# Optimization experiments

Hardware: AMD Instinct MI355X
Metric: run time of the kernel (lower is better)

## Reference

```python
import jax, jax.numpy as jnp
import numpy as np

DX = 1.0
DY = 1.0
W_DIV = 1e9
W_SMOOTH = 10.0
W_STD = 100.0
EPS = 1e-10


def _corner(a, i, j, k):
    # slice dims 2,3,4: 0 -> [0:-1], 1 -> [1:]
    sl = lambda b: slice(1, None) if b else slice(0, -1)
    return a[:, :, sl(i), sl(j), sl(k)]


def setup_inputs() -> dict:
    key = jax.random.key(0)
    k1, k2 = jax.random.split(key)
    outputs = jax.random.normal(k1, (2, 1, 256, 256, 64), dtype=jnp.float32)
    targets = jax.random.normal(k2, (2, 3, 256, 256, 64), dtype=jnp.float32)
    return {"outputs": outputs, "targets": targets}


def _loss(outputs, targets):
    bx, by, bz = targets[:, 0:1], targets[:, 1:2], targets[:, 2:3]
    z = outputs[:, 0:1]

    # vertical thickness and smoothness of its square
    dz = z[..., 1:] - z[..., :-1]
    dz2 = dz ** 2
    lap = (6 * dz2[:, :, 1:-1, 1:-1, 1:-1]
           - dz2[:, :, :-2, 1:-1, 1:-1] - dz2[:, :, 2:, 1:-1, 1:-1]
           - dz2[:, :, 1:-1, :-2, 1:-1] - dz2[:, :, 1:-1, 2:, 1:-1]
           - dz2[:, :, 1:-1, 1:-1, 2:] - dz2[:, :, 1:-1, 1:-1, :-2])
    loss_smooth = jnp.mean(lap ** 2)

    # per-(batch, channel, z) std over the spatial plane (unbiased, matching torch.std)
    loss_std = jnp.mean(jnp.std(dz, axis=(2, 3), ddof=1))

    # 8 cell corners for each field
    corners = lambda a: {(i, j, k): _corner(a, i, j, k)
                         for i in (0, 1) for j in (0, 1) for k in (0, 1)}
    BX, BY, BZ, Z = corners(bx), corners(by), corners(bz), corners(z)

    az = lambda a, b: jnp.abs(Z[a] - Z[b])
    num = (0.25 * (BX[1,0,0] + BX[1,1,0] + BX[1,0,1] + BX[1,1,1]) * DY * 0.5 * (az((1,0,1),(1,0,0)) + az((1,1,1),(1,1,0)))
           - 0.25 * (BX[0,0,0] + BX[0,1,0] + BX[0,0,1] + BX[0,1,1]) * DY * 0.5 * (az((0,0,1),(0,0,0)) + az((0,1,1),(0,1,0)))
           + 0.25 * (BY[0,1,0] + BY[1,1,0] + BY[0,1,1] + BY[1,1,1]) * DX * 0.5 * (az((0,1,1),(0,1,0)) + az((1,1,1),(1,1,0)))
           - 0.25 * (BY[0,0,0] + BY[1,0,0] + BY[0,0,1] + BY[1,0,1]) * DX * 0.5 * (az((0,0,1),(0,0,0)) + az((1,0,1),(1,0,0)))
           + 0.25 * (BZ[0,0,1] + BZ[0,1,1] + BZ[1,0,1] + BZ[1,1,1]) * DX * DY
           - 0.25 * (BZ[0,0,0] + BZ[0,1,0] + BZ[1,0,0] + BZ[1,1,0]) * DX * DY
           + (BX[0,0,1] + BX[1,0,1] + BX[1,1,1]) * DY * (Z[0,0,1] - Z[1,0,1]) / 6
           + (BX[0,1,1] + BX[1,1,1] + BX[1,0,1]) * DY * (Z[0,1,1] - Z[1,1,1]) / 6
           + (BY[1,0,1] + BY[1,1,1] + BY[0,1,1]) * DX * (Z[1,0,1] - Z[1,1,1]) / 6
           + (BY[0,0,1] + BY[0,1,1] + BY[1,1,1]) * DX * (Z[0,0,1] - Z[0,1,1]) / 6
           - (BX[0,0,0] + BX[1,0,0] + BX[1,1,0]) * DY * (Z[0,0,0] - Z[1,0,0]) / 6
           - (BX[0,1,0] + BX[1,1,0] + BX[1,0,0]) * DY * (Z[0,1,0] - Z[1,1,0]) / 6
           - (BY[1,0,0] + BY[1,1,0] + BY[0,1,0]) * DX * (Z[1,0,0] - Z[1,1,0]) / 6
           - (BY[0,0,0] + BY[0,1,0] + BY[1,1,0]) * DX * (Z[0,0,0] - Z[0,1,0]) / 6)

    sum8 = lambda C: sum(C.values())
    den = ((sum8(BX) * 0.125) ** 2 + (sum8(BY) * 0.125) ** 2
           + (sum8(BZ) * 0.125) ** 2 + EPS)
    loss_div = jnp.mean(num ** 2 / den)

    return loss_div * W_DIV, loss_smooth * W_SMOOTH + loss_std * W_STD


def reference(outputs, targets):
    return _loss(outputs, targets)
```

## Files before the change

kernel.cpp:

```cpp
#include <hip/hip_runtime.h>
#include <math.h>


__global__ __launch_bounds__(512) void zero_ws_kernel(float* ws) {
    for (int i = threadIdx.x; i < 32 * 258; i += 512) ws[i] = 0.0f;
}

__global__ __launch_bounds__(256, 4) void fused_loss_kernel(
    const float* __restrict__ zin, const float* __restrict__ tg,
    float* __restrict__ ws)
{
    __shared__ float r1[4][64];
    __shared__ float r2[4][64];
    __shared__ float rsc[4][2];

    const int tid  = threadIdx.x;
    const int lane = tid & 63;
    const int w    = tid >> 6;

    const int bb   = blockIdx.x >> 14;
    const int rest = blockIdx.x & 16383;
    const int tx   = rest & 127;
    const int ty   = rest >> 7;
    const int x    = (tx << 1) | (w >> 1);
    const int y    = (ty << 1) | (w & 1);

    const int xp = x < 255 ? x + 1 : 255;
    const int yp = y < 255 ? y + 1 : 255;
    const int xm = x > 0 ? x - 1 : 0;
    const int ym = y > 0 ? y - 1 : 0;

    const int o00 = x  * 16384 + y  * 64 + lane;
    const int o10 = xp * 16384 + y  * 64 + lane;
    const int o01 = x  * 16384 + yp * 64 + lane;
    const int o11 = xp * 16384 + yp * 64 + lane;

    const float* zb = zin + ((size_t)bb << 22);
    float zC  = zb[o00];
    float zE  = zb[o10];
    float zN  = zb[o01];
    float zNE = zb[o11];
    float zW  = zb[xm * 16384 + y * 64 + lane];
    float zS  = zb[x * 16384 + ym * 64 + lane];

    const float* tbx = tg + (((size_t)bb * 3) << 22);
    const float* tby = tbx + 4194304;
    const float* tbz = tbx + 8388608;
    float bx00 = tbx[o00], bx10 = tbx[o10], bx01 = tbx[o01], bx11 = tbx[o11];
    float by00 = tby[o00], by10 = tby[o10], by01 = tby[o01], by11 = tby[o11];
    float bz00 = tbz[o00], bz10 = tbz[o10], bz01 = tbz[o01], bz11 = tbz[o11];

    float zCp  = __shfl_down(zC,  1, 64);
    float zEp  = __shfl_down(zE,  1, 64);
    float zNp  = __shfl_down(zN,  1, 64);
    float zNEp = __shfl_down(zNE, 1, 64);
    float zWp  = __shfl_down(zW,  1, 64);
    float zSp  = __shfl_down(zS,  1, 64);

    float dz   = zCp  - zC;
    float dzE  = zEp  - zE;
    float dzN  = zNp  - zN;
    float dzNE = zNEp - zNE;
    float dzW  = zWp  - zW;
    float dzS  = zSp  - zS;

    float dzm = __shfl_up(dz, 1, 64);
    float dzp = __shfl_down(dz, 1, 64);

    float s1 = (lane < 63) ? dz : 0.0f;
    float s2 = (lane < 63) ? dz * dz : 0.0f;

    float sm = 0.0f;
    if (x >= 1 && x <= 254 && y >= 1 && y <= 254 && lane >= 1 && lane <= 61) {
        float lap = 6.0f * dz * dz
                  - dzW * dzW - dzE * dzE
                  - dzS * dzS - dzN * dzN
                  - dzm * dzm - dzp * dzp;
        sm = lap * lap;
    }

    float dv = 0.0f;
    if (x < 255 && y < 255) {
        float bxA = bx00 + bx01;
        float bxB = bx10 + bx11;
        float bxC = bxB + bx00;
        float bxD = bxB + bx01;
        float byQ = by00 + by10;
        float byP = by01 + by11;
        float byR = byP + by10;
        float byS = byP + by00;
        float bzT = ((bz00 + bz10) + bz01) + bz11;

        float bxAp = __shfl_down(bxA, 1, 64);
        float bxBp = __shfl_down(bxB, 1, 64);
        float bxCp = __shfl_down(bxC, 1, 64);
        float bxDp = __shfl_down(bxD, 1, 64);
        float byQp = __shfl_down(byQ, 1, 64);
        float byPp = __shfl_down(byP, 1, 64);
        float byRp = __shfl_down(byR, 1, 64);
        float bySp = __shfl_down(byS, 1, 64);
        float bzTp = __shfl_down(bzT, 1, 64);

        if (lane < 63) {
            float adz00 = fabsf(dz),  adz10 = fabsf(dzE);
            float adz01 = fabsf(dzN), adz11 = fabsf(dzNE);

            float num =
                0.125f * ( (bxB + bxBp) * (adz10 + adz11)
                         - (bxA + bxAp) * (adz00 + adz01)
                         + (byP + byPp) * (adz01 + adz11)
                         - (byQ + byQp) * (adz00 + adz10) )
              + 0.25f * ( bzTp - bzT );

            const float c6 = 1.0f / 6.0f;
            num += c6 * ( bxCp * (zCp - zEp)
                        + bxDp * (zNp - zNEp)
                        + byRp * (zEp - zNEp)
                        + bySp * (zCp - zNp)
                        - bxC * (zC - zE)
                        - bxD * (zN - zNE)
                        - byR * (zE - zNE)
                        - byS * (zC - zN) );

            float sbx = (bxA + bxB) + (bxAp + bxBp);
            float sby = (byQ + byP) + (byQp + byPp);
            float sbz = bzT + bzTp;
            float den = 0.015625f * (sbx * sbx + sby * sby + sbz * sbz) + 1e-10f;
            dv = num * num / den;
        }
    }

    #pragma unroll
    for (int off = 32; off > 0; off >>= 1) {
        sm += __shfl_down(sm, off, 64);
        dv += __shfl_down(dv, off, 64);
    }
    r1[w][lane] = s1;
    r2[w][lane] = s2;
    if (lane == 0) { rsc[w][0] = sm; rsc[w][1] = dv; }
    __syncthreads();

    if (tid < 64) {
        float a   = r1[0][tid] + r1[1][tid] + r1[2][tid] + r1[3][tid];
        float b2r = r2[0][tid] + r2[1][tid] + r2[2][tid] + r2[3][tid];
        float* sl = ws + (blockIdx.x & 31) * 258;
        if (tid < 63) {
            atomicAdd(&sl[2 + bb * 64 + tid],   a);
            atomicAdd(&sl[130 + bb * 64 + tid], b2r);
        }
        if (tid == 0) atomicAdd(&sl[0], rsc[0][0] + rsc[1][0] + rsc[2][0] + rsc[3][0]);
        if (tid == 1) atomicAdd(&sl[1], rsc[0][1] + rsc[1][1] + rsc[2][1] + rsc[3][1]);
    }
}

__global__ __launch_bounds__(128) void finalize_kernel(const float* __restrict__ ws,
                                                       float* __restrict__ out)
{
    __shared__ double red[128];
    const int t = threadIdx.x;
    double stdv = 0.0;
    {
        int k = t & 63, bb = t >> 6;
        if (k < 63) {
            double s1 = 0.0, s2 = 0.0;
            for (int p = 0; p < 32; ++p) {
                s1 += (double)ws[p * 258 + 2 + bb * 64 + k];
                s2 += (double)ws[p * 258 + 130 + bb * 64 + k];
            }
            const double N = 65536.0;
            double var = (s2 - s1 * s1 / N) / (N - 1.0);
            stdv = sqrt(var > 0.0 ? var : 0.0);
        }
    }
    red[t] = stdv;
    __syncthreads();
    for (int off = 64; off > 0; off >>= 1) {
        if (t < off) red[t] += red[t + off];
        __syncthreads();
    }
    if (t == 0) {
        double smt = 0.0, dvt = 0.0;
        for (int p = 0; p < 32; ++p) {
            smt += (double)ws[p * 258 + 0];
            dvt += (double)ws[p * 258 + 1];
        }
        double loss_std    = red[0] / 126.0;
        double loss_smooth = smt / (2.0 * 254.0 * 254.0 * 61.0);
        double loss_div    = dvt / (2.0 * 255.0 * 255.0 * 63.0);
        out[0] = (float)(loss_div * 1e9);
        out[1] = (float)(loss_smooth * 10.0 + loss_std * 100.0);
    }
}

extern "C" void kernel_launch(void* const* d_in, const int* in_sizes, int n_in,
                              void* d_out, int out_size, void* d_ws, size_t ws_size,
                              hipStream_t stream) {
    const float* z  = (const float*)d_in[0];
    const float* tg = (const float*)d_in[1];
    float* out = (float*)d_out;
    float* ws  = (float*)d_ws;

    zero_ws_kernel<<<1, 512, 0, stream>>>(ws);
    fused_loss_kernel<<<32768, 256, 0, stream>>>(z, tg, ws);
    finalize_kernel<<<1, 128, 0, stream>>>(ws, out);
}
```

Baseline: 181.9 us.

## Process two z-levels per thread with float2 loads and halve the grid

Each thread now handles two consecutive z entries of a column, loading all fields as float2, and each wavefront covers two y columns. The grid is halved to 16384 blocks, so per-block atomics and reduction overhead are spread over twice the work. Neighbour-in-z values now come partly from registers and partly from shuffles. The cost is higher register pressure per thread and more complex boundary handling for the second z element.

```diff
diff --git a/kernel.cpp b/kernel.cpp
--- a/kernel.cpp
+++ b/kernel.cpp
@@ -10,123 +10,162 @@
     const float* __restrict__ zin, const float* __restrict__ tg,
     float* __restrict__ ws)
 {
-    __shared__ float r1[4][64];
-    __shared__ float r2[4][64];
+    __shared__ float r1[4][2][64];
+    __shared__ float r2[4][2][64];
     __shared__ float rsc[4][2];
 
     const int tid  = threadIdx.x;
     const int lane = tid & 63;
     const int w    = tid >> 6;
-
-    const int bb   = blockIdx.x >> 14;
-    const int rest = blockIdx.x & 16383;
-    const int tx   = rest & 127;
-    const int ty   = rest >> 7;
-    const int x    = (tx << 1) | (w >> 1);
-    const int y    = (ty << 1) | (w & 1);
+    const int j    = lane & 31;
+    const int h    = lane >> 5;
+
+    const int bb   = blockIdx.x >> 13;
+    const int rest = blockIdx.x & 8191;
+    const int X    = rest & 63;
+    const int Y    = rest >> 6;
+    const int x    = (X << 2) | w;
+    const int y    = (Y << 1) | h;
+    const int k0   = j << 1;
 
     const int xp = x < 255 ? x + 1 : 255;
     const int yp = y < 255 ? y + 1 : 255;
     const int xm = x > 0 ? x - 1 : 0;
     const int ym = y > 0 ? y - 1 : 0;
 
-    const int o00 = x  * 16384 + y  * 64 + lane;
-    const int o10 = xp * 16384 + y  * 64 + lane;
-    const int o01 = x  * 16384 + yp * 64 + lane;
-    const int o11 = xp * 16384 + yp * 64 + lane;
+    const int o00 = x  * 16384 + y  * 64 + k0;
+    const int o10 = xp * 16384 + y  * 64 + k0;
+    const int o01 = x  * 16384 + yp * 64 + k0;
+    const int o11 = xp * 16384 + yp * 64 + k0;
 
     const float* zb = zin + ((size_t)bb << 22);
-    float zC  = zb[o00];
-    float zE  = zb[o10];
-    float zN  = zb[o01];
-    float zNE = zb[o11];
-    float zW  = zb[xm * 16384 + y * 64 + lane];
-    float zS  = zb[x * 16384 + ym * 64 + lane];
+    float2 zC  = *(const float2*)&zb[o00];
+    float2 zE  = *(const float2*)&zb[o10];
+    float2 zN  = *(const float2*)&zb[o01];
+    float2 zNE = *(const float2*)&zb[o11];
+    float2 zW  = *(const float2*)&zb[xm * 16384 + y * 64 + k0];
+    float2 zS  = *(const float2*)&zb[x * 16384 + ym * 64 + k0];
 
     const float* tbx = tg + (((size_t)bb * 3) << 22);
     const float* tby = tbx + 4194304;
     const float* tbz = tbx + 8388608;
-    float bx00 = tbx[o00], bx10 = tbx[o10], bx01 = tbx[o01], bx11 = tbx[o11];
-    float by00 = tby[o00], by10 = tby[o10], by01 = tby[o01], by11 = tby[o11];
-    float bz00 = tbz[o00], bz10 = tbz[o10], bz01 = tbz[o01], bz11 = tbz[o11];
-
-    float zCp  = __shfl_down(zC,  1, 64);
-    float zEp  = __shfl_down(zE,  1, 64);
-    float zNp  = __shfl_down(zN,  1, 64);
-    float zNEp = __shfl_down(zNE, 1, 64);
-    float zWp  = __shfl_down(zW,  1, 64);
-    float zSp  = __shfl_down(zS,  1, 64);
-
-    float dz   = zCp  - zC;
-    float dzE  = zEp  - zE;
-    float dzN  = zNp  - zN;
-    float dzNE = zNEp - zNE;
-    float dzW  = zWp  - zW;
-    float dzS  = zSp  - zS;
-
-    float dzm = __shfl_up(dz, 1, 64);
-    float dzp = __shfl_down(dz, 1, 64);
-
-    float s1 = (lane < 63) ? dz : 0.0f;
-    float s2 = (lane < 63) ? dz * dz : 0.0f;
+    float2 bx00 = *(const float2*)&tbx[o00], bx10 = *(const float2*)&tbx[o10];
+    float2 bx01 = *(const float2*)&tbx[o01], bx11 = *(const float2*)&tbx[o11];
+    float2 by00 = *(const float2*)&tby[o00], by10 = *(const float2*)&tby[o10];
+    float2 by01 = *(const float2*)&tby[o01], by11 = *(const float2*)&tby[o11];
+    float2 bz00 = *(const float2*)&tbz[o00], bz10 = *(const float2*)&tbz[o10];
+    float2 bz01 = *(const float2*)&tbz[o01], bz11 = *(const float2*)&tbz[o11];
+
+    float zCn  = __shfl_down(zC.x,  1, 64);
+    float zEn  = __shfl_down(zE.x,  1, 64);
+    float zNn  = __shfl_down(zN.x,  1, 64);
+    float zNEn = __shfl_down(zNE.x, 1, 64);
+    float zWn  = __shfl_down(zW.x,  1, 64);
+    float zSn  = __shfl_down(zS.x,  1, 64);
+
+    float dzC0  = zC.y  - zC.x,  dzC1  = zCn  - zC.y;
+    float dzE0  = zE.y  - zE.x,  dzE1  = zEn  - zE.y;
+    float dzN0  = zN.y  - zN.x,  dzN1  = zNn  - zN.y;
+    float dzNE0 = zNE.y - zNE.x, dzNE1 = zNEn - zNE.y;
+    float dzW0  = zW.y  - zW.x,  dzW1  = zWn  - zW.y;
+    float dzS0  = zS.y  - zS.x,  dzS1  = zSn  - zS.y;
+
+    float dzm0 = __shfl_up(dzC1, 1, 64);
+    float dzp1 = __shfl_down(dzC0, 1, 64);
+
+    float s10 = dzC0,               s20 = dzC0 * dzC0;
+    float s11 = (j < 31) ? dzC1 : 0.0f;
+    float s21 = (j < 31) ? dzC1 * dzC1 : 0.0f;
 
     float sm = 0.0f;
-    if (x >= 1 && x <= 254 && y >= 1 && y <= 254 && lane >= 1 && lane <= 61) {
-        float lap = 6.0f * dz * dz
-                  - dzW * dzW - dzE * dzE
-                  - dzS * dzS - dzN * dzN
-                  - dzm * dzm - dzp * dzp;
-        sm = lap * lap;
+    if (x >= 1 && x <= 254) {
+        bool yok = (y >= 1 && y <= 254);
+        if (yok && j >= 1 && j <= 30) {
+            float lap = 6.0f * dzC0 * dzC0
+                      - dzW0 * dzW0 - dzE0 * dzE0
+                      - dzS0 * dzS0 - dzN0 * dzN0
+                      - dzm0 * dzm0 - dzC1 * dzC1;
+            sm += lap * lap;
+        }
+        if (yok && j <= 30) {
+            float lap = 6.0f * dzC1 * dzC1
+                      - dzW1 * dzW1 - dzE1 * dzE1
+                      - dzS1 * dzS1 - dzN1 * dzN1
+                      - dzC0 * dzC0 - dzp1 * dzp1;
+            sm += lap * lap;
+        }
     }
 
     float dv = 0.0f;
-    if (x < 255 && y < 255) {
-        float bxA = bx00 + bx01;
-        float bxB = bx10 + bx11;
-        float bxC = bxB + bx00;
-        float bxD = bxB + bx01;
-        float byQ = by00 + by10;
-        float byP = by01 + by11;
-        float byR = byP + by10;
-        float byS = byP + by00;
-        float bzT = ((bz00 + bz10) + bz01) + bz11;
-
-        float bxAp = __shfl_down(bxA, 1, 64);
-        float bxBp = __shfl_down(bxB, 1, 64);
-        float bxCp = __shfl_down(bxC, 1, 64);
-        float bxDp = __shfl_down(bxD, 1, 64);
-        float byQp = __shfl_down(byQ, 1, 64);
-        float byPp = __shfl_down(byP, 1, 64);
-        float byRp = __shfl_down(byR, 1, 64);
-        float bySp = __shfl_down(byS, 1, 64);
-        float bzTp = __shfl_down(bzT, 1, 64);
-
-        if (lane < 63) {
-            float adz00 = fabsf(dz),  adz10 = fabsf(dzE);
-            float adz01 = fabsf(dzN), adz11 = fabsf(dzNE);
-
+    if (x < 255) {
+        float bxA0 = bx00.x + bx01.x, bxA1 = bx00.y + bx01.y;
+        float bxB0 = bx10.x + bx11.x, bxB1 = bx10.y + bx11.y;
+        float bxC0 = bxB0 + bx00.x,  bxC1 = bxB1 + bx00.y;
+        float bxD0 = bxB0 + bx01.x,  bxD1 = bxB1 + bx01.y;
+        float byQ0 = by00.x + by10.x, byQ1 = by00.y + by10.y;
+        float byP0 = by01.x + by11.x, byP1 = by01.y + by11.y;
+        float byR0 = byP0 + by10.x,  byR1 = byP1 + by10.y;
+        float byS0 = byP0 + by00.x,  byS1 = byP1 + by00.y;
+        float bzT0 = ((bz00.x + bz10.x) + bz01.x) + bz11.x;
+        float bzT1 = ((bz00.y + bz10.y) + bz01.y) + bz11.y;
+
+        float bxAs = __shfl_down(bxA0, 1, 64);
+        float bxBs = __shfl_down(bxB0, 1, 64);
+        float bxCs = __shfl_down(bxC0, 1, 64);
+        float bxDs = __shfl_down(bxD0, 1, 64);
+        float byQs = __shfl_down(byQ0, 1, 64);
+        float byPs = __shfl_down(byP0, 1, 64);
+        float byRs = __shfl_down(byR0, 1, 64);
+        float bySs = __shfl_down(byS0, 1, 64);
+        float bzTs = __shfl_down(bzT0, 1, 64);
+
+        const float c6 = 1.0f / 6.0f;
+        if (y < 255) {
+            float adz00 = fabsf(dzC0), adz10 = fabsf(dzE0);
+            float adz01 = fabsf(dzN0), adz11 = fabsf(dzNE0);
             float num =
-                0.125f * ( (bxB + bxBp) * (adz10 + adz11)
-                         - (bxA + bxAp) * (adz00 + adz01)
-                         + (byP + byPp) * (adz01 + adz11)
-                         - (byQ + byQp) * (adz00 + adz10) )
-              + 0.25f * ( bzTp - bzT );
-
-            const float c6 = 1.0f / 6.0f;
-            num += c6 * ( bxCp * (zCp - zEp)
-                        + bxDp * (zNp - zNEp)
-                        + byRp * (zEp - zNEp)
-                        + bySp * (zCp - zNp)
-                        - bxC * (zC - zE)
-                        - bxD * (zN - zNE)
-                        - byR * (zE - zNE)
-                        - byS * (zC - zN) );
-
-            float sbx = (bxA + bxB) + (bxAp + bxBp);
-            float sby = (byQ + byP) + (byQp + byPp);
-            float sbz = bzT + bzTp;
+                0.125f * ( (bxB0 + bxB1) * (adz10 + adz11)
+                         - (bxA0 + bxA1) * (adz00 + adz01)
+                         + (byP0 + byP1) * (adz01 + adz11)
+                         - (byQ0 + byQ1) * (adz00 + adz10) )
+              + 0.25f * ( bzT1 - bzT0 );
+            num += c6 * ( bxC1 * (zC.y - zE.y)
+                        + bxD1 * (zN.y - zNE.y)
+                        + byR1 * (zE.y - zNE.y)
+                        + byS1 * (zC.y - zN.y)
+                        - bxC0 * (zC.x - zE.x)
+                        - bxD0 * (zN.x - zNE.x)
+                        - byR0 * (zE.x - zNE.x)
+                        - byS0 * (zC.x - zN.x) );
+            float sbx = (bxA0 + bxB0) + (bxA1 + bxB1);
+            float sby = (byQ0 + byP0) + (byQ1 + byP1);
+            float sbz = bzT0 + bzT1;
             float den = 0.015625f * (sbx * sbx + sby * sby + sbz * sbz) + 1e-10f;
             dv = num * num / den;
+
+            if (j < 31) {
+                float a00 = fabsf(dzC1), a10 = fabsf(dzE1);
+                float a01 = fabsf(dzN1), a11 = fabsf(dzNE1);
+                float num1 =
+                    0.125f * ( (bxB1 + bxBs) * (a10 + a11)
+                             - (bxA1 + bxAs) * (a00 + a01)
+                             + (byP1 + byPs) * (a01 + a11)
+                             - (byQ1 + byQs) * (a00 + a10) )
+                  + 0.25f * ( bzTs - bzT1 );
+                num1 += c6 * ( bxCs * (zCn - zEn)
+                             + bxDs * (zNn - zNEn)
+                             + byRs * (zEn - zNEn)
+                             + bySs * (zCn - zNn)
+                             - bxC1 * (zC.y - zE.y)
+                             - bxD1 * (zN.y - zNE.y)
+                             - byR1 * (zE.y - zNE.y)
+                             - byS1 * (zC.y - zN.y) );
+                float sbx1 = (bxA1 + bxB1) + (bxAs + bxBs);
+                float sby1 = (byQ1 + byP1) + (byQs + byPs);
+                float sbz1 = bzT1 + bzTs;
+                float den1 = 0.015625f * (sbx1 * sbx1 + sby1 * sby1 + sbz1 * sbz1) + 1e-10f;
+                dv += num1 * num1 / den1;
+            }
         }
     }
 
@@ -135,14 +174,16 @@
         sm += __shfl_down(sm, off, 64);
         dv += __shfl_down(dv, off, 64);
     }
-    r1[w][lane] = s1;
-    r2[w][lane] = s2;
+    { float2 v; v.x = s10; v.y = s11; *(float2*)&r1[w][h][k0] = v; }
+    { float2 v; v.x = s20; v.y = s21; *(float2*)&r2[w][h][k0] = v; }
     if (lane == 0) { rsc[w][0] = sm; rsc[w][1] = dv; }
     __syncthreads();
 
     if (tid < 64) {
-        float a   = r1[0][tid] + r1[1][tid] + r1[2][tid] + r1[3][tid];
-        float b2r = r2[0][tid] + r2[1][tid] + r2[2][tid] + r2[3][tid];
+        float a   = ((r1[0][0][tid] + r1[0][1][tid]) + (r1[1][0][tid] + r1[1][1][tid]))
+                  + ((r1[2][0][tid] + r1[2][1][tid]) + (r1[3][0][tid] + r1[3][1][tid]));
+        float b2r = ((r2[0][0][tid] + r2[0][1][tid]) + (r2[1][0][tid] + r2[1][1][tid]))
+                  + ((r2[2][0][tid] + r2[2][1][tid]) + (r2[3][0][tid] + r2[3][1][tid]));
         float* sl = ws + (blockIdx.x & 31) * 258;
         if (tid < 63) {
             atomicAdd(&sl[2 + bb * 64 + tid],   a);
@@ -201,6 +242,6 @@
     float* ws  = (float*)d_ws;
 
     zero_ws_kernel<<<1, 512, 0, stream>>>(ws);
-    fused_loss_kernel<<<32768, 256, 0, stream>>>(z, tg, ws);
+    fused_loss_kernel<<<16384, 256, 0, stream>>>(z, tg, ws);
     finalize_kernel<<<1, 128, 0, stream>>>(ws, out);
 }
```

After: 198.3 us. +9.0%, slower.
